# Optimization experiments

Measured on AMD Instinct MI355X. Metric: run time of the kernel, lower is better.

## Reference

```python
import jax, jax.numpy as jnp
import numpy as np

HID = 7168; H = 128; DQ = 1536; DKV = 512; DH = 128; DR = 64; MAXS = 4096

def _rope_tables(seq_len):
    inv_freq = 1.0 / (10000.0 ** (jnp.arange(0, DR, 2, dtype=jnp.float32) / DR))
    t = jnp.arange(seq_len, dtype=jnp.float32)
    freqs = jnp.outer(t, inv_freq)              # [S, DR/2]
    emb = jnp.concatenate([freqs, freqs], -1)   # [S, DR]
    return jnp.cos(emb), jnp.sin(emb)

def _apply_rope(x, cos, sin):
    # x: [..., S, DR]; cos/sin: [S, DR]
    d = x.shape[-1]
    x1, x2 = x[..., : d // 2], x[..., d // 2 :]
    rotated = jnp.concatenate([-x2, x1], -1)
    return (x * cos + rotated * sin).astype(x.dtype)

def setup_inputs() -> dict:
    key = jax.random.key(0)
    ks = jax.random.split(key, 16)
    s = 0.02
    inp = {
        "h":    jax.random.normal(ks[0], (1, 1024, HID), jnp.float32),
        "Wdq":  jax.random.normal(ks[1], (DQ, HID), jnp.float32) * s,
        "bdq":  jnp.zeros((DQ,), jnp.float32),
        "Wdkv": jax.random.normal(ks[2], (DKV, HID), jnp.float32) * s,
        "bdkv": jnp.zeros((DKV,), jnp.float32),
        "Wuq":  jax.random.normal(ks[3], (H * DH, DQ), jnp.float32) * s,
        "buq":  jnp.zeros((H * DH,), jnp.float32),
        "Wukv": jax.random.normal(ks[4], (H * DH * 2, DKV), jnp.float32) * s,
        "bukv": jnp.zeros((H * DH * 2,), jnp.float32),
        "Wrq":  jax.random.normal(ks[5], (H * DR, DQ), jnp.float32) * s,
        "brq":  jnp.zeros((H * DR,), jnp.float32),
        "Wrk":  jax.random.normal(ks[6], (DR, HID), jnp.float32) * s,
        "brk":  jnp.zeros((DR,), jnp.float32),
        "Wo":   jax.random.normal(ks[7], (HID, H * DH), jnp.float32) * s,
        "bo":   jnp.zeros((HID,), jnp.float32),
    }
    return inp

def reference(h, Wdq, bdq, Wdkv, bdkv, Wuq, buq, Wukv, bukv, Wrq, brq, Wrk, brk, Wo, bo):
    B, S, _ = h.shape
    c_q = h @ Wdq.T + bdq              # [B,S,DQ]
    c_kv = h @ Wdkv.T + bdkv           # [B,S,DKV]
    q_c = (c_q @ Wuq.T + buq).reshape(B, S, H, DH).transpose(0, 2, 1, 3)     # [B,H,S,DH]
    kv_c = (c_kv @ Wukv.T + bukv).reshape(B, S, H, 2 * DH).transpose(0, 2, 1, 3)
    k_c, v = kv_c[..., :DH], kv_c[..., DH:]                                  # [B,H,S,DH]
    q_r = (c_q @ Wrq.T + brq).reshape(B, S, H, DR).transpose(0, 2, 1, 3)     # [B,H,S,DR]
    k_r = (h @ Wrk.T + brk).reshape(B, S, 1, DR).transpose(0, 2, 1, 3)       # [B,1,S,DR]
    cos, sin = _rope_tables(S)
    q_r = _apply_rope(q_r, cos, sin)
    k_r = _apply_rope(k_r, cos, sin)
    q = jnp.concatenate([q_c, q_r], -1)                                      # [B,H,S,DH+DR]
    k = jnp.concatenate([k_c, jnp.broadcast_to(k_r, (B, H, S, DR))], -1)
    scale = 1.0 / jnp.sqrt(jnp.float32(DH + DR))
    scores = jnp.einsum('bhqd,bhkd->bhqk', q, k) * scale
    attn = jax.nn.softmax(scores, axis=-1)
    o = jnp.einsum('bhqk,bhkd->bhqd', attn, v)        # [B,H,S,DH]
    o = o.transpose(0, 2, 1, 3).reshape(B, S, H * DH)
    return o @ Wo.T + bo
```

## Files before the change

kernel.cpp:

```cpp
#include <hip/hip_runtime.h>
#include <hip/hip_bf16.h>

#define S_LEN 1024
#define HID 7168
#define NH 128
#define DQ 1536
#define DKV 512
#define DH 128
#define DR 64

typedef __attribute__((ext_vector_type(8))) short bf16x8;
typedef __attribute__((ext_vector_type(4))) float f32x4;
typedef __attribute__((ext_vector_type(4))) float fl4;
typedef __attribute__((ext_vector_type(4))) unsigned short us4;
typedef __attribute__((ext_vector_type(8))) unsigned short us8;
typedef __attribute__((ext_vector_type(4))) unsigned int u32x4;

static __device__ __forceinline__ unsigned short f2bf(float f) {
  union { float f; unsigned int u; } v; v.f = f;
  unsigned int u = v.u;
  return (unsigned short)((u + 0x7fffu + ((u >> 16) & 1u)) >> 16);
}
static __device__ __forceinline__ float bf2f(unsigned short u) {
  union { unsigned int u; float f; } v; v.u = ((unsigned int)u) << 16;
  return v.f;
}
static __device__ __forceinline__ unsigned int cvtpk2(float lo, float hi) {
  unsigned int r;
  asm("v_cvt_pk_bf16_f32 %0, %1, %2" : "=v"(r) : "v"(lo), "v"(hi));
  return r;
}

__global__ __launch_bounds__(256) void cvt_bf16_kernel(
    const float* __restrict__ in, unsigned short* __restrict__ out, int n8) {
  int i = blockIdx.x * 256 + threadIdx.x;
  int stride = gridDim.x * 256;
  for (; i < n8; i += stride) {
    fl4 a = ((const fl4*)in)[2 * i];
    fl4 b = ((const fl4*)in)[2 * i + 1];
    us8 u = { f2bf(a[0]), f2bf(a[1]), f2bf(a[2]), f2bf(a[3]),
              f2bf(b[0]), f2bf(b[1]), f2bf(b[2]), f2bf(b[3]) };
    ((us8*)out)[i] = u;
  }
}

template <int OUTMODE, int WFP32, int ROPEQ = 0>
__global__ __launch_bounds__(256) void gemm_k(
    const unsigned short* __restrict__ A, int lda,
    const unsigned short* __restrict__ Wb16,
    const float* __restrict__ Wfa, const float* __restrict__ Wfb, int nsplit,
    int ldw,
    const float* __restrict__ bias,
    void* __restrict__ Cv, int ldc, size_t zstride,
    int Ncl, int ksl, float alpha,
    const float* __restrict__ ctab = nullptr,
    const float* __restrict__ stab = nullptr)
{
  const int n0 = blockIdx.x * 128;
  if (n0 >= Ncl) return;

  __shared__ unsigned short As[128 * 64];
  __shared__ unsigned short Ws[128 * 64];
  const int t = threadIdx.x;
  const int l = t & 63, w = t >> 6;
  const int r15 = l & 15, g = l >> 4;
  const int wm = (w >> 1) * 64, wn = (w & 1) * 64;
  const int m0 = blockIdx.y * 128;
  const int kbase = blockIdx.z * ksl;
  const int srow = l >> 3;
  const int scol = (l & 7) * 8;

  f32x4 acc[4][4];
#pragma unroll
  for (int i = 0; i < 4; ++i)
#pragma unroll
    for (int j = 0; j < 4; ++j) acc[i][j] = (f32x4){0.f, 0.f, 0.f, 0.f};

  const unsigned short* Ab = A + (size_t)m0 * lda;
  const unsigned short* Wb = nullptr;
  const float* Wf = nullptr;
  if constexpr (WFP32) {
    Wf = (n0 < nsplit) ? Wfa + (size_t)n0 * ldw : Wfb + (size_t)(n0 - nsplit) * ldw;
  } else {
    Wb = Wb16 + (size_t)n0 * ldw;
  }

  fl4 wx[4], wy[4];
  auto issueW = [&](int k0) {
#pragma unroll
    for (int i = 0; i < 4; ++i) {
      int c = t + 256 * i;
      const float* src = Wf + (size_t)(c >> 3) * ldw + k0 + (c & 7) * 8;
      wx[i] = *(const fl4*)src;
      wy[i] = *(const fl4*)(src + 4);
    }
  };

  if constexpr (WFP32) issueW(kbase);
  const int kend = kbase + ksl;

  for (int k0 = kbase; k0 < kend; k0 += 64) {
    if constexpr (WFP32) {
      __builtin_amdgcn_s_barrier();
      __builtin_amdgcn_sched_barrier(0);
    } else {
      __syncthreads();
    }
#pragma unroll
    for (int i = 0; i < 4; ++i) {
      int chunk = w * 4 + i;
      int row = chunk * 8 + srow;
      __builtin_amdgcn_global_load_lds(
          (const __attribute__((address_space(1))) void*)(Ab + (size_t)row * lda + k0 + scol),
          (__attribute__((address_space(3))) void*)(As + chunk * 512), 16, 0, 0);
      if constexpr (!WFP32) {
        __builtin_amdgcn_global_load_lds(
            (const __attribute__((address_space(1))) void*)(Wb + (size_t)row * ldw + k0 + scol),
            (__attribute__((address_space(3))) void*)(Ws + chunk * 512), 16, 0, 0);
      }
    }
    if constexpr (WFP32) {
      __builtin_amdgcn_sched_barrier(0);
      asm volatile("s_waitcnt vmcnt(4)" ::: "memory");
      __builtin_amdgcn_sched_barrier(0);
#pragma unroll
      for (int i = 0; i < 4; ++i) {
        int c = t + 256 * i;
        u32x4 p = { cvtpk2(wx[i][0], wx[i][1]), cvtpk2(wx[i][2], wx[i][3]),
                    cvtpk2(wy[i][0], wy[i][1]), cvtpk2(wy[i][2], wy[i][3]) };
        ((u32x4*)Ws)[c] = p;
      }
      if (k0 + 64 < kend) {
        issueW(k0 + 64);
        __builtin_amdgcn_sched_barrier(0);
        asm volatile("s_waitcnt vmcnt(8) lgkmcnt(0)" ::: "memory");
      } else {
        asm volatile("s_waitcnt vmcnt(0) lgkmcnt(0)" ::: "memory");
      }
      __builtin_amdgcn_sched_barrier(0);
      __builtin_amdgcn_s_barrier();
    } else {
      __syncthreads();
    }
#pragma unroll
    for (int kk = 0; kk < 2; ++kk) {
      bf16x8 a[4], b[4];
#pragma unroll
      for (int mt = 0; mt < 4; ++mt)
        a[mt] = *reinterpret_cast<const bf16x8*>(&As[(wm + mt * 16 + r15) * 64 + kk * 32 + 8 * g]);
#pragma unroll
      for (int nt = 0; nt < 4; ++nt)
        b[nt] = *reinterpret_cast<const bf16x8*>(&Ws[(wn + nt * 16 + r15) * 64 + kk * 32 + 8 * g]);
#pragma unroll
      for (int mt = 0; mt < 4; ++mt)
#pragma unroll
        for (int nt = 0; nt < 4; ++nt)
          acc[mt][nt] = __builtin_amdgcn_mfma_f32_16x16x32_bf16(a[mt], b[nt], acc[mt][nt], 0, 0, 0);
    }
  }

  if constexpr (OUTMODE == 1) {
    float bv[4];
#pragma unroll
    for (int nt = 0; nt < 4; ++nt) {
      int col = n0 + wn + nt * 16 + r15;
      bv[nt] = (col < Ncl) ? bias[col] : 0.f;
    }
    bool isrope = false;
    if constexpr (ROPEQ) isrope = (n0 + wn) >= 16384;
    if (ROPEQ && isrope) {
#pragma unroll
      for (int mt = 0; mt < 4; ++mt)
#pragma unroll
        for (int r = 0; r < 4; ++r) {
          int row = m0 + wm + mt * 16 + g * 4 + r;
#pragma unroll
          for (int ntp = 0; ntp < 2; ++ntp) {
            int j = ntp * 16 + r15;
            float c = ctab[row * 32 + j];
            float s = stab[row * 32 + j];
            float x1 = acc[mt][ntp][r] + bv[ntp];
            float x2 = acc[mt][ntp + 2][r] + bv[ntp + 2];
            int col1 = n0 + wn + ntp * 16 + r15;
            ((unsigned short*)Cv)[(size_t)row * ldc + col1] =
                f2bf((x1 * c - x2 * s) * alpha);
            ((unsigned short*)Cv)[(size_t)row * ldc + col1 + 32] =
                f2bf((x2 * c + x1 * s) * alpha);
          }
        }
    } else {
#pragma unroll
      for (int mt = 0; mt < 4; ++mt)
#pragma unroll
        for (int nt = 0; nt < 4; ++nt) {
          int col = n0 + wn + nt * 16 + r15;
          if (col < Ncl) {
#pragma unroll
            for (int r = 0; r < 4; ++r) {
              int row = m0 + wm + mt * 16 + g * 4 + r;
              ((unsigned short*)Cv)[(size_t)row * ldc + col] =
                  f2bf((acc[mt][nt][r] + bv[nt]) * alpha);
            }
          }
        }
    }
  } else {
    float* Cp = (float*)Cv + blockIdx.z * zstride;
#pragma unroll
    for (int mt = 0; mt < 4; ++mt)
#pragma unroll
      for (int nt = 0; nt < 4; ++nt) {
        int col = n0 + wn + nt * 16 + r15;
        if (col < Ncl) {
#pragma unroll
          for (int r = 0; r < 4; ++r) {
            int row = m0 + wm + mt * 16 + g * 4 + r;
            Cp[(size_t)row * ldc + col] = acc[mt][nt][r];
          }
        }
      }
  }
}

#define G4_DSREAD_A(buf, mh)                                                  \
  _Pragma("unroll") for (int mf = 0; mf < 4; ++mf)                            \
  _Pragma("unroll") for (int kk = 0; kk < 2; ++kk)                            \
    af[mf][kk] = rdA(buf, mh, mf, kk);

#define G4_DSREAD_B(buf, nh, breg)                                            \
  _Pragma("unroll") for (int nf = 0; nf < 2; ++nf)                            \
  _Pragma("unroll") for (int kk = 0; kk < 2; ++kk)                            \
    breg[nf][kk] = rdB(buf, nh, nf, kk);

#define G4_MFMA(mh, nh, breg)                                                 \
  __builtin_amdgcn_s_setprio(1);                                              \
  _Pragma("unroll") for (int kk = 0; kk < 2; ++kk)                            \
  _Pragma("unroll") for (int mf = 0; mf < 4; ++mf)                            \
  _Pragma("unroll") for (int nf = 0; nf < 2; ++nf)                            \
    acc[mh][nh][mf][nf] = __builtin_amdgcn_mfma_f32_16x16x32_bf16(            \
        af[mf][kk], breg[nf][kk], acc[mh][nh][mf][nf], 0, 0, 0);              \
  __builtin_amdgcn_s_setprio(0);

#define G4_BAR_IN()                                                           \
  __builtin_amdgcn_s_barrier();                                               \
  asm volatile("s_waitcnt lgkmcnt(0)" ::: "memory");                          \
  __builtin_amdgcn_sched_barrier(0);

#define G4_BAR_OUT()                                                          \
  __builtin_amdgcn_sched_barrier(0);                                          \
  __builtin_amdgcn_s_barrier();

__global__ __launch_bounds__(512, 2) void gemm_g4_8ph(
    const unsigned short* __restrict__ A,
    const unsigned short* __restrict__ W,
    float* __restrict__ pbuf)
{
  __shared__ unsigned short S[65536];
  const int t = threadIdx.x;
  const int l = t & 63, w = t >> 6;
  const int r15 = l & 15, g = l >> 4;
  const int n0 = blockIdx.x * 256;
  const int m0 = blockIdx.y * 256;
  const int kbase = blockIdx.z * 4096;
  const int NT = 64;

  const int lp = (l & 56) | ((l ^ (l >> 3)) & 7);
  const int srow = lp >> 3;
  const int scol = (lp & 7) * 8;
  const int pr = (w >> 2) * 64;
  const int pc = (w & 3) * 32;

  f32x4 acc[2][2][4][2];
#pragma unroll
  for (int a0 = 0; a0 < 2; ++a0)
#pragma unroll
    for (int a1 = 0; a1 < 2; ++a1)
#pragma unroll
      for (int a2 = 0; a2 < 4; ++a2)
#pragma unroll
        for (int a3 = 0; a3 < 2; ++a3)
          acc[a0][a1][a2][a3] = (f32x4){0.f, 0.f, 0.f, 0.f};

  auto stage = [&](int tile, int which) {
    if (tile >= NT) return;
    const int k0 = kbase + tile * 64;
    const unsigned short* gb = (which < 2)
        ? A + (size_t)(m0 + which * 128) * 16384 + k0
        : W + (size_t)(n0 + (which - 2) * 128) * 16384 + k0;
    unsigned short* dst = S + (tile & 1) * 32768 + which * 8192;
#pragma unroll
    for (int i = 0; i < 2; ++i) {
      __builtin_amdgcn_global_load_lds(
          (const __attribute__((address_space(1))) void*)(gb + (size_t)((w * 2 + i) * 8 + srow) * 16384 + scol),
          (__attribute__((address_space(3))) void*)(dst + (w * 2 + i) * 512 + l * 8), 16, 0, 0);
    }
  };

  auto rdA = [&](int buf, int mh, int mf, int kk) -> bf16x8 {
    int row = pr + mf * 16 + r15;
    int L = row * 128 + kk * 64 + g * 16;
    L ^= ((L >> 7) & 7) << 4;
    return *(const bf16x8*)((const char*)S + buf * 65536 + mh * 16384 + L);
  };
  auto rdB = [&](int buf, int nh, int nf, int kk) -> bf16x8 {
    int row = pc + nf * 16 + r15;
    int L = row * 128 + kk * 64 + g * 16;
    L ^= ((L >> 7) & 7) << 4;
    return *(const bf16x8*)((const char*)S + buf * 65536 + (2 + nh) * 16384 + L);
  };

  bf16x8 af[4][2], bA[2][2], bB[2][2];

  stage(0, 0); stage(0, 1); stage(0, 2); stage(0, 3);
  stage(1, 0); stage(1, 2); stage(1, 3);
  __builtin_amdgcn_sched_barrier(0);
  asm volatile("s_waitcnt vmcnt(6)" ::: "memory");
  __builtin_amdgcn_sched_barrier(0);
  __builtin_amdgcn_s_barrier();

  for (int i = 0; i < 32; ++i) {
    const int tb = 2 * i;
    const bool last = (i == 31);
    G4_DSREAD_A(0, 0)
    G4_DSREAD_B(0, 0, bA)
    stage(tb + 1, 1);
    G4_BAR_IN()
    G4_MFMA(0, 0, bA)
    G4_BAR_OUT()
    G4_DSREAD_B(0, 1, bB)
    stage(tb + 2, 0);
    G4_BAR_IN()
    G4_MFMA(0, 1, bB)
    G4_BAR_OUT()
    G4_DSREAD_A(0, 1)
    stage(tb + 2, 2);
    G4_BAR_IN()
    G4_MFMA(1, 1, bB)
    G4_BAR_OUT()
    stage(tb + 2, 3);
    G4_BAR_IN()
    G4_MFMA(1, 0, bA)
    if (last) { asm volatile("s_waitcnt vmcnt(0)" ::: "memory"); }
    else      { asm volatile("s_waitcnt vmcnt(6)" ::: "memory"); }
    G4_BAR_OUT()
    G4_DSREAD_A(1, 0)
    G4_DSREAD_B(1, 0, bA)
    stage(tb + 2, 1);
    G4_BAR_IN()
    G4_MFMA(0, 0, bA)
    G4_BAR_OUT()
    G4_DSREAD_B(1, 1, bB)
    stage(tb + 3, 0);
    G4_BAR_IN()
    G4_MFMA(0, 1, bB)
    G4_BAR_OUT()
    G4_DSREAD_A(1, 1)
    stage(tb + 3, 2);
    G4_BAR_IN()
    G4_MFMA(1, 1, bB)
    G4_BAR_OUT()
    stage(tb + 3, 3);
    G4_BAR_IN()
    G4_MFMA(1, 0, bA)
    if (last) { asm volatile("s_waitcnt vmcnt(0)" ::: "memory"); }
    else      { asm volatile("s_waitcnt vmcnt(6)" ::: "memory"); }
    G4_BAR_OUT()
  }

  float* Cp = pbuf + (size_t)blockIdx.z * 1024 * 7168;
#pragma unroll
  for (int mh = 0; mh < 2; ++mh)
#pragma unroll
    for (int nh = 0; nh < 2; ++nh)
#pragma unroll
      for (int mf = 0; mf < 4; ++mf)
#pragma unroll
        for (int nf = 0; nf < 2; ++nf) {
          int col = n0 + nh * 128 + pc + nf * 16 + r15;
#pragma unroll
          for (int r = 0; r < 4; ++r) {
            int row = m0 + mh * 128 + pr + mf * 16 + g * 4 + r;
            Cp[(size_t)row * 7168 + col] = acc[mh][nh][mf][nf][r];
          }
        }
}

__global__ __launch_bounds__(256) void reduce_f32_kernel(
    const float* __restrict__ pbuf, const float* __restrict__ bias,
    float* __restrict__ out, int ldo, int rowlen4, int nz, size_t zstride, int total4)
{
  int idx = blockIdx.x * 256 + threadIdx.x;
  if (idx >= total4) return;
  int r = idx / rowlen4, c4 = idx % rowlen4;
  fl4 acc = *(const fl4*)(bias + c4 * 4);
  for (int z = 0; z < nz; ++z)
    acc += *(const fl4*)(pbuf + z * zstride + (size_t)idx * 4);
  *(fl4*)(out + (size_t)r * ldo + c4 * 4) = acc;
}

__global__ __launch_bounds__(256) void reduce_bf16_kernel(
    const float* __restrict__ pbuf, const float* __restrict__ bias,
    unsigned short* __restrict__ out, int ldo, int rowlen4, int nz, size_t zstride, int total4)
{
  int idx = blockIdx.x * 256 + threadIdx.x;
  if (idx >= total4) return;
  int r = idx / rowlen4, c4 = idx % rowlen4;
  fl4 acc = *(const fl4*)(bias + c4 * 4);
  for (int z = 0; z < nz; ++z)
    acc += *(const fl4*)(pbuf + z * zstride + (size_t)idx * 4);
  us4 u = { f2bf(acc[0]), f2bf(acc[1]), f2bf(acc[2]), f2bf(acc[3]) };
  *(us4*)(out + (size_t)r * ldo + c4 * 4) = u;
}

__global__ __launch_bounds__(256) void rope_table_kernel(float* __restrict__ ctab,
                                                         float* __restrict__ stab) {
  int idx = blockIdx.x * 256 + threadIdx.x;
  if (idx >= S_LEN * 32) return;
  int j = idx & 31, s = idx >> 5;
  float invf = expf(-0.28782313662425574f * (float)j);
  float ang = (float)s * invf;
  ctab[idx] = cosf(ang);
  stab[idx] = sinf(ang);
}

__global__ void rope_bf16_kernel(unsigned short* __restrict__ x, int nh, int lda, int total,
                                 const float* __restrict__ ctab,
                                 const float* __restrict__ stab) {
  int idx = blockIdx.x * 256 + threadIdx.x;
  if (idx >= total) return;
  int j = idx & 31;
  int rest = idx >> 5;
  int hh = rest % nh;
  int s = rest / nh;
  float c = ctab[s * 32 + j], sn = stab[s * 32 + j];
  size_t base = (size_t)s * lda + hh * 64;
  float x1 = bf2f(x[base + j]), x2 = bf2f(x[base + j + 32]);
  x[base + j]      = f2bf(x1 * c - x2 * sn);
  x[base + j + 32] = f2bf(x2 * c + x1 * sn);
}

__global__ __launch_bounds__(256) void vtrans_kernel(
    const unsigned short* __restrict__ kvb, unsigned short* __restrict__ vt) {
  __shared__ unsigned short tl[64][72];
  const int s0 = blockIdx.x * 64;
  const int c0 = blockIdx.y * 64;
  const int t = threadIdx.x;
  const int rr = t >> 3, cc = (t & 7) * 8;
  const int hbase = (c0 >> 7) * 256 + 128 + (c0 & 127);
#pragma unroll
  for (int i = 0; i < 2; ++i) {
    int r = rr + i * 32;
    *reinterpret_cast<bf16x8*>(&tl[r][cc]) =
        *reinterpret_cast<const bf16x8*>(kvb + (size_t)(s0 + r) * 32768 + hbase + cc);
  }
  __syncthreads();
#pragma unroll
  for (int i = 0; i < 2; ++i) {
    int vc = rr + i * 32;
    unsigned short tmp[8];
#pragma unroll
    for (int j = 0; j < 8; ++j) tmp[j] = tl[cc + j][vc];
    *reinterpret_cast<bf16x8*>(&vt[(size_t)(c0 + vc) * 1024 + s0 + cc]) =
        *reinterpret_cast<bf16x8*>(tmp);
  }
}

__global__ __launch_bounds__(512) void mla_attn_kernel(
    const unsigned short* __restrict__ qcat,
    const unsigned short* __restrict__ kvb,
    const unsigned short* __restrict__ kr,
    const unsigned short* __restrict__ vt,
    unsigned short* __restrict__ obuf)
{
  __shared__ unsigned short Klds[64][200];
  __shared__ unsigned short Vlds[128][72];
  __shared__ unsigned short Plds[8][16][72];

  const int t = threadIdx.x;
  const int l = t & 63, w = t >> 6;
  const int r15 = l & 15, g = l >> 4;
  const int bid = blockIdx.x;
  const int orig = (bid & 7) * 128 + (bid >> 3);
  const int h = orig >> 3;
  const int q0 = (orig & 7) * 128;

  bf16x8 qf[6];
  const unsigned short* qrow = qcat + (size_t)(q0 + w * 16 + r15) * 24576;
#pragma unroll
  for (int kk = 0; kk < 4; ++kk)
    qf[kk] = *reinterpret_cast<const bf16x8*>(qrow + h * 128 + kk * 32 + 8 * g);
#pragma unroll
  for (int kk = 4; kk < 6; ++kk)
    qf[kk] = *reinterpret_cast<const bf16x8*>(qrow + 16384 + h * 64 + (kk - 4) * 32 + 8 * g);

  bf16x8 kreg[3], vreg[2];
  auto loadKV = [&](int kk0) {
#pragma unroll
    for (int i = 0; i < 3; ++i) {
      int c = t + 512 * i, row = c / 24, cb = c % 24;
      const unsigned short* src = (cb < 16)
          ? kvb + (size_t)(kk0 + row) * 32768 + h * 256 + cb * 8
          : kr + (size_t)(kk0 + row) * 2112 + (cb - 16) * 8;
      kreg[i] = *reinterpret_cast<const bf16x8*>(src);
    }
#pragma unroll
    for (int i = 0; i < 2; ++i) {
      int c = t + 512 * i, d = c >> 3, kb = c & 7;
      vreg[i] = *reinterpret_cast<const bf16x8*>(vt + ((size_t)h * 128 + d) * 1024 + kk0 + kb * 8);
    }
  };

  float m_r[4], l_r[4];
  f32x4 oacc[8];
#pragma unroll
  for (int r = 0; r < 4; ++r) { m_r[r] = -1e30f; l_r[r] = 0.f; }
#pragma unroll
  for (int d = 0; d < 8; ++d) oacc[d] = (f32x4){0.f, 0.f, 0.f, 0.f};

  loadKV(0);

  for (int kt = 0; kt < 16; ++kt) {
    __syncthreads();
#pragma unroll
    for (int i = 0; i < 3; ++i) {
      int c = t + 512 * i, row = c / 24, cb = c % 24;
      *reinterpret_cast<bf16x8*>(&Klds[row][cb * 8]) = kreg[i];
    }
#pragma unroll
    for (int i = 0; i < 2; ++i) {
      int c = t + 512 * i, d = c >> 3, kb = c & 7;
      *reinterpret_cast<bf16x8*>(&Vlds[d][kb * 8]) = vreg[i];
    }
    __syncthreads();
    if (kt < 15) loadKV((kt + 1) * 64);

    f32x4 sacc[4];
#pragma unroll
    for (int nt = 0; nt < 4; ++nt) sacc[nt] = (f32x4){0.f, 0.f, 0.f, 0.f};
    __builtin_amdgcn_s_setprio(1);
#pragma unroll
    for (int nt = 0; nt < 4; ++nt)
#pragma unroll
      for (int kk = 0; kk < 6; ++kk) {
        bf16x8 b = *reinterpret_cast<const bf16x8*>(&Klds[nt * 16 + r15][kk * 32 + 8 * g]);
        sacc[nt] = __builtin_amdgcn_mfma_f32_16x16x32_bf16(qf[kk], b, sacc[nt], 0, 0, 0);
      }
    __builtin_amdgcn_s_setprio(0);

    float mx[4];
#pragma unroll
    for (int r = 0; r < 4; ++r) {
      float m = fmaxf(fmaxf(sacc[0][r], sacc[1][r]), fmaxf(sacc[2][r], sacc[3][r]));
      m = fmaxf(m, __shfl_xor(m, 1));
      m = fmaxf(m, __shfl_xor(m, 2));
      m = fmaxf(m, __shfl_xor(m, 4));
      m = fmaxf(m, __shfl_xor(m, 8));
      mx[r] = m;
    }
    float grow = fmaxf(fmaxf(mx[0] - m_r[0], mx[1] - m_r[1]),
                       fmaxf(mx[2] - m_r[2], mx[3] - m_r[3]));
    if (__any(grow > 8.0f)) {
      float sc[4];
#pragma unroll
      for (int r = 0; r < 4; ++r) {
        float mn = fmaxf(m_r[r], mx[r]);
        sc[r] = __expf(m_r[r] - mn);
        m_r[r] = mn;
        l_r[r] *= sc[r];
      }
#pragma unroll
      for (int d = 0; d < 8; ++d)
#pragma unroll
        for (int r = 0; r < 4; ++r) oacc[d][r] *= sc[r];
    }
    float rsum[4] = {0.f, 0.f, 0.f, 0.f};
#pragma unroll
    for (int nt = 0; nt < 4; ++nt)
#pragma unroll
      for (int r = 0; r < 4; ++r) {
        float p = __expf(sacc[nt][r] - m_r[r]);
        rsum[r] += p;
        Plds[w][g * 4 + r][nt * 16 + r15] = f2bf(p);
      }
#pragma unroll
    for (int r = 0; r < 4; ++r) {
      float s = rsum[r];
      s += __shfl_xor(s, 1);
      s += __shfl_xor(s, 2);
      s += __shfl_xor(s, 4);
      s += __shfl_xor(s, 8);
      l_r[r] += s;
    }

    bf16x8 pa0 = *reinterpret_cast<const bf16x8*>(&Plds[w][r15][8 * g]);
    bf16x8 pa1 = *reinterpret_cast<const bf16x8*>(&Plds[w][r15][32 + 8 * g]);
    __builtin_amdgcn_s_setprio(1);
#pragma unroll
    for (int dt = 0; dt < 8; ++dt) {
      bf16x8 v0 = *reinterpret_cast<const bf16x8*>(&Vlds[dt * 16 + r15][8 * g]);
      bf16x8 v1 = *reinterpret_cast<const bf16x8*>(&Vlds[dt * 16 + r15][32 + 8 * g]);
      oacc[dt] = __builtin_amdgcn_mfma_f32_16x16x32_bf16(pa0, v0, oacc[dt], 0, 0, 0);
      oacc[dt] = __builtin_amdgcn_mfma_f32_16x16x32_bf16(pa1, v1, oacc[dt], 0, 0, 0);
    }
    __builtin_amdgcn_s_setprio(0);
  }

#pragma unroll
  for (int dt = 0; dt < 8; ++dt)
#pragma unroll
    for (int r = 0; r < 4; ++r) {
      int row = q0 + w * 16 + g * 4 + r;
      int col = h * DH + dt * 16 + r15;
      obuf[(size_t)row * 16384 + col] = f2bf(oacc[dt][r] / l_r[r]);
    }
}

extern "C" void kernel_launch(void* const* d_in, const int* in_sizes, int n_in,
                              void* d_out, int out_size, void* d_ws, size_t ws_size,
                              hipStream_t stream) {
  const float* h    = (const float*)d_in[0];
  const float* Wdq  = (const float*)d_in[1];
  const float* bdq  = (const float*)d_in[2];
  const float* Wdkv = (const float*)d_in[3];
  const float* bdkv = (const float*)d_in[4];
  const float* Wuq  = (const float*)d_in[5];
  const float* buq  = (const float*)d_in[6];
  const float* Wukv = (const float*)d_in[7];
  const float* bukv = (const float*)d_in[8];
  const float* Wrq  = (const float*)d_in[9];
  const float* brq  = (const float*)d_in[10];
  const float* Wrk  = (const float*)d_in[11];
  const float* brk  = (const float*)d_in[12];
  const float* Wo   = (const float*)d_in[13];
  const float* bo   = (const float*)d_in[14];
  float* out = (float*)d_out;

  char* ws = (char*)d_ws;
  size_t off = 0;
  auto alloc = [&](size_t bytes) {
    char* p = ws + off;
    off += (bytes + 255) & ~(size_t)255;
    return p;
  };
  unsigned short* hb    = (unsigned short*)alloc((size_t)1024 * 7168 * 2);
  unsigned short* W1cat = (unsigned short*)alloc((size_t)2176 * 7168 * 2);
  float*          b1cat = (float*)alloc(2176 * 4);
  float*          b2cat = (float*)alloc(24576 * 4);
  unsigned short* ccat  = (unsigned short*)alloc((size_t)1024 * 2112 * 2);
  unsigned short* qcat  = (unsigned short*)alloc((size_t)1024 * 24576 * 2);
  unsigned short* kvbb  = (unsigned short*)alloc((size_t)1024 * 32768 * 2);
  unsigned short* vt    = (unsigned short*)alloc((size_t)16384 * 1024 * 2);
  unsigned short* obuf  = (unsigned short*)alloc((size_t)1024 * 16384 * 2);
  float*          ctab  = (float*)alloc((size_t)S_LEN * 32 * 4);
  float*          stab  = (float*)alloc((size_t)S_LEN * 32 * 4);
  unsigned short* Wukvb = (unsigned short*)alloc((size_t)32768 * 512 * 2);
  float* pbufG1 = (float*)qcat;
  unsigned short* Wob    = (unsigned short*)(ws + ((size_t)288 << 20));
  float*          pbufG4 = (float*)(ws + ((size_t)544 << 20));

  auto cvt = [&](const float* in, unsigned short* outp, size_t n) {
    int n8 = (int)(n / 8);
    int blocks = (n8 + 255) / 256;
    if (blocks > 2048) blocks = 2048;
    cvt_bf16_kernel<<<blocks, 256, 0, stream>>>(in, outp, n8);
  };

  cvt(h,    hb,    (size_t)1024 * 7168);
  cvt(Wdq,  W1cat, (size_t)1536 * 7168);
  cvt(Wdkv, W1cat + (size_t)1536 * 7168, (size_t)512 * 7168);
  cvt(Wrk,  W1cat + (size_t)2048 * 7168, (size_t)64 * 7168);
  cvt(Wukv, Wukvb, (size_t)32768 * 512);
  hipMemsetAsync(W1cat + (size_t)2112 * 7168, 0, (size_t)64 * 7168 * 2, stream);
  hipMemcpyAsync(b1cat,        bdq,  1536 * 4, hipMemcpyDeviceToDevice, stream);
  hipMemcpyAsync(b1cat + 1536, bdkv, 512 * 4,  hipMemcpyDeviceToDevice, stream);
  hipMemcpyAsync(b1cat + 2048, brk,  64 * 4,   hipMemcpyDeviceToDevice, stream);
  hipMemsetAsync(b1cat + 2112, 0, 64 * 4, stream);
  hipMemcpyAsync(b2cat,         buq, 16384 * 4, hipMemcpyDeviceToDevice, stream);
  hipMemcpyAsync(b2cat + 16384, brq, 8192 * 4,  hipMemcpyDeviceToDevice, stream);
  rope_table_kernel<<<(S_LEN * 32 + 255) / 256, 256, 0, stream>>>(ctab, stab);

  const float scale = 0.07216878364870323f;
  const int BIGN = 1 << 30;
  dim3 blk(256);

  gemm_k<2, 0><<<dim3(24, 8, 4), blk, 0, stream>>>(
      hb, 7168, W1cat, nullptr, nullptr, BIGN, 7168, nullptr,
      pbufG1, 2112, (size_t)1024 * 2112, 2112, 1792, 1.0f);
  reduce_bf16_kernel<<<2112, blk, 0, stream>>>(pbufG1, b1cat, ccat, 2112, 528, 4,
                                               (size_t)1024 * 2112, 1024 * 2112 / 4);
  rope_bf16_kernel<<<(1024 * 32 + 255) / 256, blk, 0, stream>>>(ccat + 2048, 1, 2112, 1024 * 32, ctab, stab);

  gemm_k<1, 1, 1><<<dim3(192, 8, 1), blk, 0, stream>>>(
      ccat, 2112, nullptr, Wuq, Wrq, 16384, 1536, b2cat,
      qcat, 24576, 0, 24576, 1536, scale, ctab, stab);

  gemm_k<1, 0><<<dim3(256, 8, 1), blk, 0, stream>>>(
      ccat + 1536, 2112, Wukvb, nullptr, nullptr, BIGN, 512, bukv,
      kvbb, 32768, 0, 32768, 512, 1.0f);
  vtrans_kernel<<<dim3(16, 256), blk, 0, stream>>>(kvbb, vt);
  mla_attn_kernel<<<dim3(1024), dim3(512), 0, stream>>>(qcat, kvbb, ccat + 2048, vt, obuf);

  cvt(Wo, Wob, (size_t)7168 * 16384);
  gemm_g4_8ph<<<dim3(28, 4, 4), dim3(512), 0, stream>>>(obuf, Wob, pbufG4);
  reduce_f32_kernel<<<7168, blk, 0, stream>>>(pbufG4, bo, out,
                                              7168, 1792, 4, (size_t)1024 * 7168, 1024 * 7168 / 4);
}
```

Before: 976.2 us.

## Merge setup conversions into fused kernels and halve output GEMM split-K

The five separate fp32-to-bf16 conversion launches are replaced by a single cvt5_kernel. The memset and memcpy bias-concatenation calls are replaced by one setup_kernel. This is meant to cut launch and API overhead between small operations. Separately, the output projection GEMM moves from split-K 4 to split-K 2 with twice the K-loop length, so the final reduction reads half as many partial buffers, at the cost of fewer workgroups (224 vs 448) in that GEMM.

```diff
diff --git a/kernel.cpp b/kernel.cpp
--- a/kernel.cpp
+++ b/kernel.cpp
@@ -42,6 +42,56 @@
               f2bf(b[0]), f2bf(b[1]), f2bf(b[2]), f2bf(b[3]) };
     ((us8*)out)[i] = u;
   }
+}
+
+__global__ __launch_bounds__(256) void cvt5_kernel(
+    const float* __restrict__ h,    const float* __restrict__ wdq,
+    const float* __restrict__ wdkv, const float* __restrict__ wrk,
+    const float* __restrict__ wukv,
+    unsigned short* __restrict__ hb, unsigned short* __restrict__ w1cat,
+    unsigned short* __restrict__ wukvb)
+{
+  const int s0 = 917504;
+  const int s1 = s0 + 1376256;
+  const int s2 = s1 + 458752;
+  const int s3 = s2 + 57344;
+  const int s4 = s3 + 2097152;
+  int i = blockIdx.x * 256 + threadIdx.x;
+  int stride = gridDim.x * 256;
+  for (; i < s4; i += stride) {
+    const float* src;
+    unsigned short* dst;
+    int j;
+    if (i < s0)      { src = h;    dst = hb;                              j = i; }
+    else if (i < s1) { src = wdq;  dst = w1cat;                           j = i - s0; }
+    else if (i < s2) { src = wdkv; dst = w1cat + (size_t)1536 * 7168;     j = i - s1; }
+    else if (i < s3) { src = wrk;  dst = w1cat + (size_t)2048 * 7168;     j = i - s2; }
+    else             { src = wukv; dst = wukvb;                           j = i - s3; }
+    fl4 a = ((const fl4*)src)[2 * j];
+    fl4 b = ((const fl4*)src)[2 * j + 1];
+    us8 u = { f2bf(a[0]), f2bf(a[1]), f2bf(a[2]), f2bf(a[3]),
+              f2bf(b[0]), f2bf(b[1]), f2bf(b[2]), f2bf(b[3]) };
+    ((us8*)dst)[j] = u;
+  }
+}
+
+__global__ __launch_bounds__(256) void setup_kernel(
+    const float* __restrict__ bdq, const float* __restrict__ bdkv,
+    const float* __restrict__ brk, const float* __restrict__ buq,
+    const float* __restrict__ brq,
+    float* __restrict__ b1cat, float* __restrict__ b2cat,
+    unsigned short* __restrict__ w1pad)
+{
+  int i = blockIdx.x * 256 + threadIdx.x;
+  if (i < 458752) w1pad[i] = 0;
+  if (i < 2176) {
+    float v = (i < 1536) ? bdq[i]
+            : (i < 2048) ? bdkv[i - 1536]
+            : (i < 2112) ? brk[i - 2048] : 0.f;
+    b1cat[i] = v;
+  }
+  if (i < 24576)
+    b2cat[i] = (i < 16384) ? buq[i] : brq[i - 16384];
 }
 
 template <int OUTMODE, int WFP32, int ROPEQ = 0>
@@ -261,8 +311,8 @@
   const int r15 = l & 15, g = l >> 4;
   const int n0 = blockIdx.x * 256;
   const int m0 = blockIdx.y * 256;
-  const int kbase = blockIdx.z * 4096;
-  const int NT = 64;
+  const int kbase = blockIdx.z * 8192;
+  const int NT = 128;
 
   const int lp = (l & 56) | ((l ^ (l >> 3)) & 7);
   const int srow = lp >> 3;
@@ -318,9 +368,9 @@
   __builtin_amdgcn_sched_barrier(0);
   __builtin_amdgcn_s_barrier();
 
-  for (int i = 0; i < 32; ++i) {
+  for (int i = 0; i < 64; ++i) {
     const int tb = 2 * i;
-    const bool last = (i == 31);
+    const bool last = (i == 63);
     G4_DSREAD_A(0, 0)
     G4_DSREAD_B(0, 0, bA)
     stage(tb + 1, 1);
@@ -658,30 +708,14 @@
   unsigned short* Wob    = (unsigned short*)(ws + ((size_t)288 << 20));
   float*          pbufG4 = (float*)(ws + ((size_t)544 << 20));
 
-  auto cvt = [&](const float* in, unsigned short* outp, size_t n) {
-    int n8 = (int)(n / 8);
-    int blocks = (n8 + 255) / 256;
-    if (blocks > 2048) blocks = 2048;
-    cvt_bf16_kernel<<<blocks, 256, 0, stream>>>(in, outp, n8);
-  };
-
-  cvt(h,    hb,    (size_t)1024 * 7168);
-  cvt(Wdq,  W1cat, (size_t)1536 * 7168);
-  cvt(Wdkv, W1cat + (size_t)1536 * 7168, (size_t)512 * 7168);
-  cvt(Wrk,  W1cat + (size_t)2048 * 7168, (size_t)64 * 7168);
-  cvt(Wukv, Wukvb, (size_t)32768 * 512);
-  hipMemsetAsync(W1cat + (size_t)2112 * 7168, 0, (size_t)64 * 7168 * 2, stream);
-  hipMemcpyAsync(b1cat,        bdq,  1536 * 4, hipMemcpyDeviceToDevice, stream);
-  hipMemcpyAsync(b1cat + 1536, bdkv, 512 * 4,  hipMemcpyDeviceToDevice, stream);
-  hipMemcpyAsync(b1cat + 2048, brk,  64 * 4,   hipMemcpyDeviceToDevice, stream);
-  hipMemsetAsync(b1cat + 2112, 0, 64 * 4, stream);
-  hipMemcpyAsync(b2cat,         buq, 16384 * 4, hipMemcpyDeviceToDevice, stream);
-  hipMemcpyAsync(b2cat + 16384, brq, 8192 * 4,  hipMemcpyDeviceToDevice, stream);
-  rope_table_kernel<<<(S_LEN * 32 + 255) / 256, 256, 0, stream>>>(ctab, stab);
-
   const float scale = 0.07216878364870323f;
   const int BIGN = 1 << 30;
   dim3 blk(256);
+
+  cvt5_kernel<<<2048, blk, 0, stream>>>(h, Wdq, Wdkv, Wrk, Wukv, hb, W1cat, Wukvb);
+  setup_kernel<<<1792, blk, 0, stream>>>(bdq, bdkv, brk, buq, brq,
+                                         b1cat, b2cat, W1cat + (size_t)2112 * 7168);
+  rope_table_kernel<<<(S_LEN * 32 + 255) / 256, blk, 0, stream>>>(ctab, stab);
 
   gemm_k<2, 0><<<dim3(24, 8, 4), blk, 0, stream>>>(
       hb, 7168, W1cat, nullptr, nullptr, BIGN, 7168, nullptr,
@@ -700,8 +734,8 @@
   vtrans_kernel<<<dim3(16, 256), blk, 0, stream>>>(kvbb, vt);
   mla_attn_kernel<<<dim3(1024), dim3(512), 0, stream>>>(qcat, kvbb, ccat + 2048, vt, obuf);
 
-  cvt(Wo, Wob, (size_t)7168 * 16384);
-  gemm_g4_8ph<<<dim3(28, 4, 4), dim3(512), 0, stream>>>(obuf, Wob, pbufG4);
+  cvt_bf16_kernel<<<2048, blk, 0, stream>>>(Wo, Wob, (int)((size_t)7168 * 16384 / 8));
+  gemm_g4_8ph<<<dim3(28, 4, 2), dim3(512), 0, stream>>>(obuf, Wob, pbufG4);
   reduce_f32_kernel<<<7168, blk, 0, stream>>>(pbufG4, bo, out,
-                                              7168, 1792, 4, (size_t)1024 * 7168, 1024 * 7168 / 4);
-}
+                                              7168, 1792, 2, (size_t)1024 * 7168, 1024 * 7168 / 4);
+}
```

Measured after the change: 936.3 us. -4.1%, faster.
